# Kernel optimization log

Hardware: AMD Instinct MI355X
Metric: run time of the kernel (lower is better)

The kernel has to match this reference:

```python
import jax, jax.numpy as jnp
import numpy as np

SEQ, B, IN, H = 512, 256, 300, 256

def setup_inputs() -> dict:
    key = jax.random.key(0)
    ks = jax.random.split(key, 14)
    s = lambda *sh: 1.0 / np.sqrt(sh[0])
    inp = {
        'secuencia': jax.random.normal(ks[0], (SEQ, B, IN), jnp.float32),
        # RNN cell 1 (forward direction)
        'W1x': jax.random.normal(ks[1], (IN, H), jnp.float32) * s(IN),
        'W1h': jax.random.normal(ks[2], (H, H), jnp.float32) * s(H),
        'b1':  jax.random.normal(ks[3], (H,), jnp.float32) * 0.01,
        # RNN cell 2 (backward direction)
        'W2x': jax.random.normal(ks[4], (IN, H), jnp.float32) * s(IN),
        'W2h': jax.random.normal(ks[5], (H, H), jnp.float32) * s(H),
        'b2':  jax.random.normal(ks[6], (H,), jnp.float32) * 0.01,
        # MLP head (weights stored [in, out])
        'fc1_w': jax.random.normal(ks[7], (2 * H, 2 * H), jnp.float32) * s(2 * H),
        'fc1_b': jnp.zeros((2 * H,), jnp.float32),
        'fc2_w': jax.random.normal(ks[8], (2 * H, H), jnp.float32) * s(2 * H),
        'fc2_b': jnp.zeros((H,), jnp.float32),
        'fs_w':  jax.random.normal(ks[9], (H, 1), jnp.float32) * s(H),
        'fs_b':  jnp.zeros((1,), jnp.float32),
    }
    return inp

def _rnn_scan(seq, Wx, Wh, b):
    # seq: [S, B, IN] -> final hidden [B, H]; Elman cell h' = tanh(x Wx + h Wh + b)
    h0 = jnp.zeros((seq.shape[1], Wh.shape[0]), seq.dtype)
    def step(h, x):
        return jnp.tanh(x @ Wx + h @ Wh + b), None
    h_final, _ = jax.lax.scan(step, h0, seq)
    return h_final

def reference(secuencia, W1x, W1h, b1, W2x, W2h, b2,
              fc1_w, fc1_b, fc2_w, fc2_b, fs_w, fs_b):
    h1 = _rnn_scan(secuencia, W1x, W1h, b1)          # forward pass over time
    h2 = _rnn_scan(secuencia[::-1], W2x, W2h, b2)    # reversed pass over time
    h = jnp.concatenate([h1, h2], axis=1)            # [B, 2H]
    x = jax.nn.relu(h @ fc1_w + fc1_b)
    x = jax.nn.relu(x @ fc2_w + fc2_b)
    out = jnp.tanh(x @ fs_w + fs_b)                  # [B, 1]
    return out.squeeze()
```

## Files before the change

kernel.cpp:

```cpp
#include <hip/hip_runtime.h>

#define DI __device__ __forceinline__

typedef float f32x4 __attribute__((ext_vector_type(4)));
typedef float f4    __attribute__((ext_vector_type(4)));
typedef _Float16 h8 __attribute__((ext_vector_type(8)));
typedef _Float16 h4 __attribute__((ext_vector_type(4)));

#define SEQL 512
#define BATCH 256
#define INF 300
#define HID 256
#define N2 512
#define KP 320


DI float ftanh(float x) {
    float e = __builtin_amdgcn_exp2f(x * 2.8853900817779268f);
    return fmaf(-2.0f, __builtin_amdgcn_rcpf(e + 1.0f), 1.0f);
}

__global__ void prep_kernel(const float* __restrict__ W1x, const float* __restrict__ W2x,
                            const float* __restrict__ b1, const float* __restrict__ b2,
                            _Float16* __restrict__ WTs, float* __restrict__ bcat)
{
    int idx = blockIdx.x * 256 + threadIdx.x;
    if (idx < N2 * KP) {
        int j = idx / KP, z = idx - j * KP;
        int k = z ^ ((j & 7) << 3);
        float v = 0.f;
        if (k < INF) v = (j < HID) ? W1x[k * HID + j] : W2x[k * HID + (j - HID)];
        WTs[j * KP + z] = (_Float16)v;
    }
    if (idx < N2) bcat[idx] = (idx < HID) ? b1[idx] : b2[idx - HID];
}

__global__ __launch_bounds__(512, 2) void gemm_pre(
    const float* __restrict__ x, const _Float16* __restrict__ WTs,
    const float* __restrict__ bcat, _Float16* __restrict__ pre3)
{
    __shared__ _Float16 AbD[2][128 * 64];
    __shared__ _Float16 BbD[2][256 * 64];
    const int tid = threadIdx.x;
    const int w = tid >> 6, l = tid & 63;
    const int lj = l & 15, lg = l >> 4;
    const int bid = blockIdx.x;
    const int xcd = bid & 7;
    const int idx0 = bid >> 3;
    const int jn = idx0 & 1;
    const int bm = xcd * 128 + (idx0 >> 1);
    const size_t m0 = (size_t)bm * 128;
    const int j0b = jn * 256;
    const int wj = (w >> 1) * 64, wm2 = (w & 1) * 64;

    f32x4 acc[4][4];
#pragma unroll
    for (int a = 0; a < 4; ++a)
#pragma unroll
        for (int b = 0; b < 4; ++b) acc[a][b] = f32x4{0.f, 0.f, 0.f, 0.f};

    char* Acur = (char*)AbD[0];
    char* Anxt = (char*)AbD[1];
    char* Bcur = (char*)BbD[0];
    char* Bnxt = (char*)BbD[1];

    const int amr = w * 16;

#define STAGE_W(K0, BDST)                                                             \
    do {                                                                              \
        _Pragma("unroll")                                                             \
        for (int q = 0; q < 4; ++q) {                                                 \
            int idx = q * 512 + tid;                                                  \
            int jr = idx >> 3, sl = idx & 7;                                          \
            const _Float16* src = WTs + (size_t)(j0b + jr) * KP + (K0) + sl * 8;      \
            _Float16* dst = (_Float16*)(BDST) + (size_t)(q * 512 + w * 64) * 8;       \
            __builtin_amdgcn_global_load_lds(                                         \
                (const __attribute__((address_space(1))) void*)src,                   \
                (__attribute__((address_space(3))) void*)dst, 16, 0, 0);              \
        }                                                                             \
    } while (0)

#define LOAD_X(K0, XR)                                                                \
    do {                                                                              \
        _Pragma("unroll")                                                             \
        for (int c = 0; c < 4; ++c) {                                                 \
            int f = c * 512 + tid;                                                    \
            int mr = f >> 4, k4 = f & 15;                                             \
            if ((K0) + k4 * 4 + 3 < INF)                                              \
                XR[c] = *(const f4*)(x + (m0 + mr) * INF + (K0) + k4 * 4);            \
            else                                                                      \
                XR[c] = f4{0.f, 0.f, 0.f, 0.f};                                       \
        }                                                                             \
    } while (0)

#define WRITE_X(XR, ADST)                                                             \
    do {                                                                              \
        _Pragma("unroll")                                                             \
        for (int c = 0; c < 4; ++c) {                                                 \
            int f = c * 512 + tid;                                                    \
            int mr = f >> 4, k4 = f & 15;                                             \
            unsigned bo = (unsigned)mr * 128 + (((unsigned)k4 * 8) ^ ((mr & 7) << 4)); \
            *(h4*)((ADST) + bo) = h4{(_Float16)XR[c][0], (_Float16)XR[c][1],          \
                                     (_Float16)XR[c][2], (_Float16)XR[c][3]};         \
        }                                                                             \
    } while (0)

#define GBARRIER()                                                                    \
    do {                                                                              \
        __builtin_amdgcn_sched_barrier(0);                                            \
        asm volatile("s_waitcnt vmcnt(0) lgkmcnt(0)" ::: "memory");                   \
        __builtin_amdgcn_s_barrier();                                                 \
        __builtin_amdgcn_sched_barrier(0);                                            \
    } while (0)

    {
        f4 xr[4];
        STAGE_W(0, Bcur);
        LOAD_X(0, xr);
        asm volatile("s_waitcnt vmcnt(0)" ::: "memory");
        WRITE_X(xr, Acur);
        GBARRIER();
    }

    for (int s = 0; s < 5; ++s) {
        f4 xr[4];
        if (s < 4) {
            const int k0n = (s + 1) * 64;
            STAGE_W(k0n, Bnxt);
            LOAD_X(k0n, xr);
        }
#pragma unroll
        for (int kk = 0; kk < 2; ++kk) {
            h8 aw[4], bx[4];
#pragma unroll
            for (int jt = 0; jt < 4; ++jt) {
                int jr = wj + jt * 16 + lj;
                unsigned bo = (unsigned)jr * 128 + (((unsigned)(kk * 64 + lg * 16)) ^ ((jr & 7) << 4));
                aw[jt] = *(const h8*)(Bcur + bo);
            }
#pragma unroll
            for (int mt = 0; mt < 4; ++mt) {
                int mr = wm2 + mt * 16 + lj;
                unsigned bo = (unsigned)mr * 128 + (((unsigned)(kk * 64 + lg * 16)) ^ ((mr & 7) << 4));
                bx[mt] = *(const h8*)(Acur + bo);
            }
#pragma unroll
            for (int jt = 0; jt < 4; ++jt)
#pragma unroll
                for (int mt = 0; mt < 4; ++mt)
                    acc[jt][mt] = __builtin_amdgcn_mfma_f32_16x16x32_f16(aw[jt], bx[mt], acc[jt][mt], 0, 0, 0);
        }
        if (s < 4) {
            asm volatile("s_waitcnt vmcnt(0)" ::: "memory");
            WRITE_X(xr, Anxt);
        }
        GBARRIER();
        char* t0 = Acur; Acur = Anxt; Anxt = t0;
        char* t1 = Bcur; Bcur = Bnxt; Bnxt = t1;
    }
#undef STAGE_W
#undef LOAD_X
#undef WRITE_X
#undef GBARRIER

    f4 bias4[4];
#pragma unroll
    for (int jt = 0; jt < 4; ++jt)
        bias4[jt] = *(const f4*)(bcat + j0b + wj + jt * 16 + lg * 4);
    char* prc = (char*)pre3;
#pragma unroll
    for (int jt = 0; jt < 4; ++jt) {
        int slab = (j0b + wj + jt * 16) >> 4;
#pragma unroll
        for (int mt = 0; mt < 4; ++mt) {
            int M = (int)m0 + wm2 + mt * 16;
            size_t byte = (size_t)(M >> 8) * 262144 + (size_t)slab * 8192
                        + (size_t)((M & 255) + lj) * 32 + (size_t)lg * 8;
            h4 o;
#pragma unroll
            for (int i = 0; i < 4; ++i)
                o[i] = (_Float16)(acc[jt][mt][i] + bias4[jt][i]);
            *(h4*)(prc + byte) = o;
        }
    }
    (void)amr;
}

__global__ __launch_bounds__(512, 2) void rnn_scan(
    const float* __restrict__ W1h, const float* __restrict__ W2h,
    const _Float16* __restrict__ pre3, float* __restrict__ hcat)
{
    __shared__ char hbs[16384];
    char* hbc = hbs;
    const int tid = threadIdx.x;
    const int w = tid >> 6, l = tid & 63;
    const int lj = l & 15, lg = l >> 4;
    const int dir = blockIdx.x & 1;
    const int b0 = (int)(blockIdx.x >> 1) * 16;
    const float* Wh = dir ? W2h : W1h;
    const int j0 = w * 32;
    const int dirOff = dir ? HID : 0;

    h8 afrag[2][8];
#pragma unroll
    for (int jt = 0; jt < 2; ++jt) {
        int jc = j0 + jt * 16 + lj;
#pragma unroll
        for (int kk = 0; kk < 8; ++kk) {
            h8 t;
#pragma unroll
            for (int i = 0; i < 8; ++i) t[i] = (_Float16)Wh[(kk * 32 + lg * 8 + i) * HID + jc];
            afrag[jt][kk] = t;
        }
    }

    const unsigned rb = (unsigned)l * 16;
    const unsigned wb0 = (unsigned)w * 1024 + (unsigned)(lg >> 1) * 256
                       + (unsigned)lj * 16 + (unsigned)(lg & 1) * 8;

    ((h8*)hbs)[tid] = h8{0, 0, 0, 0, 0, 0, 0, 0};
    __syncthreads();

    const long long sb = dir ? -262144LL : 262144LL;
    const char* pp = (const char*)pre3 + (long long)(dir ? (SEQL - 1) : 0) * 262144
                   + (long long)dir * 131072
                   + (long long)w * 16384 + (long long)(b0 + lj) * 32 + lg * 8;
    h4 pA[2], pB[2];
#pragma unroll
    for (int jt = 0; jt < 2; ++jt) pA[jt] = *(const h4*)(pp + jt * 8192);
    pp += sb;
#pragma unroll
    for (int jt = 0; jt < 2; ++jt) pB[jt] = *(const h4*)(pp + jt * 8192);
    pp += sb;

#define RNN_STEP(RB, WB, P, DO_PF)                                                    \
    do {                                                                              \
        h8 bf[8];                                                                     \
        _Pragma("unroll")                                                             \
        for (int kk = 0; kk < 8; ++kk)                                                \
            bf[kk] = *(const h8*)(hbc + (RB) + kk * 1024 + rb);                       \
        f32x4 acc0, acc1;                                                             \
        _Pragma("unroll")                                                             \
        for (int i = 0; i < 4; ++i) { acc0[i] = (float)P[0][i]; acc1[i] = (float)P[1][i]; } \
        if (DO_PF) {                                                                  \
            P[0] = *(const h4*)(pp);                                                  \
            P[1] = *(const h4*)(pp + 8192);                                           \
            pp += sb;                                                                 \
        }                                                                             \
        _Pragma("unroll")                                                             \
        for (int kk = 0; kk < 8; ++kk)                                                \
            acc0 = __builtin_amdgcn_mfma_f32_16x16x32_f16(afrag[0][kk], bf[kk], acc0, 0, 0, 0); \
        h4 o0;                                                                        \
        _Pragma("unroll")                                                             \
        for (int i = 0; i < 4; ++i) o0[i] = (_Float16)ftanh(acc0[i]);                 \
        *(h4*)(hbc + (WB) + wb0) = o0;                                                \
        _Pragma("unroll")                                                             \
        for (int kk = 0; kk < 8; ++kk)                                                \
            acc1 = __builtin_amdgcn_mfma_f32_16x16x32_f16(afrag[1][kk], bf[kk], acc1, 0, 0, 0); \
        h4 o1;                                                                        \
        _Pragma("unroll")                                                             \
        for (int i = 0; i < 4; ++i) o1[i] = (_Float16)ftanh(acc1[i]);                 \
        *(h4*)(hbc + (WB) + wb0 + 512) = o1;                                          \
        __builtin_amdgcn_sched_barrier(0);                                            \
        asm volatile("s_waitcnt lgkmcnt(0)" ::: "memory");                            \
        __builtin_amdgcn_s_barrier();                                                 \
        __builtin_amdgcn_sched_barrier(0);                                            \
    } while (0)

    for (int tp = 0; tp < 255; ++tp) {
        RNN_STEP(0, 8192, pA, 1);
        RNN_STEP(8192, 0, pB, 1);
    }
    RNN_STEP(0, 8192, pA, 0);

    {
        f32x4 acc0, acc1;
#pragma unroll
        for (int i = 0; i < 4; ++i) { acc0[i] = (float)pB[0][i]; acc1[i] = (float)pB[1][i]; }
        h8 bf[8];
#pragma unroll
        for (int kk = 0; kk < 8; ++kk)
            bf[kk] = *(const h8*)(hbc + 8192 + kk * 1024 + rb);
#pragma unroll
        for (int kk = 0; kk < 8; ++kk) {
            acc0 = __builtin_amdgcn_mfma_f32_16x16x32_f16(afrag[0][kk], bf[kk], acc0, 0, 0, 0);
            acc1 = __builtin_amdgcn_mfma_f32_16x16x32_f16(afrag[1][kk], bf[kk], acc1, 0, 0, 0);
        }
        f4 v0, v1;
#pragma unroll
        for (int i = 0; i < 4; ++i) { v0[i] = ftanh(acc0[i]); v1[i] = ftanh(acc1[i]); }
        float* hc = hcat + (size_t)(b0 + lj) * N2 + dirOff + j0 + lg * 4;
        *(f4*)hc = v0;
        *(f4*)(hc + 16) = v1;
    }
#undef RNN_STEP
}

__global__ __launch_bounds__(256) void head_mlp(
    const float* __restrict__ hcat,
    const float* __restrict__ fc1w, const float* __restrict__ fc1b,
    const float* __restrict__ fc2w, const float* __restrict__ fc2b,
    const float* __restrict__ fsw, const float* __restrict__ fsb,
    float* __restrict__ out)
{
    __shared__ float hs[4 * 512];
    __shared__ float y1[4 * 512];
    __shared__ float y2[4 * 256];
    const int tid = threadIdx.x;
    const int b0 = blockIdx.x * 4;
    const int r = tid >> 6;
    const int lane = tid & 63;

#pragma unroll
    for (int c = 0; c < 2; ++c)
        ((f4*)hs)[c * 256 + tid] = ((const f4*)(hcat + (size_t)b0 * N2))[c * 256 + tid];
    __syncthreads();

    {
        const int j0 = lane * 8;
        f4 a0 = *(const f4*)(fc1b + j0);
        f4 a1 = *(const f4*)(fc1b + j0 + 4);
        for (int k = 0; k < 512; ++k) {
            float h = hs[r * 512 + k];
            f4 w0 = *(const f4*)(fc1w + (size_t)k * 512 + j0);
            f4 w1 = *(const f4*)(fc1w + (size_t)k * 512 + j0 + 4);
#pragma unroll
            for (int i = 0; i < 4; ++i) { a0[i] = fmaf(h, w0[i], a0[i]); a1[i] = fmaf(h, w1[i], a1[i]); }
        }
#pragma unroll
        for (int i = 0; i < 4; ++i) {
            y1[r * 512 + j0 + i]     = fmaxf(a0[i], 0.f);
            y1[r * 512 + j0 + 4 + i] = fmaxf(a1[i], 0.f);
        }
    }
    __syncthreads();

    {
        const int j2 = lane * 4;
        f4 a = *(const f4*)(fc2b + j2);
        for (int k = 0; k < 512; ++k) {
            float yv = y1[r * 512 + k];
            f4 w = *(const f4*)(fc2w + (size_t)k * 256 + j2);
#pragma unroll
            for (int i = 0; i < 4; ++i) a[i] = fmaf(yv, w[i], a[i]);
        }
#pragma unroll
        for (int i = 0; i < 4; ++i) y2[r * 256 + j2 + i] = fmaxf(a[i], 0.f);
    }
    __syncthreads();

    {
        float p = 0.f;
#pragma unroll
        for (int u = 0; u < 4; ++u)
            p = fmaf(y2[r * 256 + lane + u * 64], fsw[lane + u * 64], p);
#pragma unroll
        for (int off = 32; off > 0; off >>= 1) p += __shfl_down(p, off);
        __shared__ float red[4];
        if ((tid & 63) == 0) red[tid >> 6] = p;
        __syncthreads();
        if (tid == 0) {
            float s = red[0] + red[1] + red[2] + red[3];
        }
        if (lane == 0) out[b0 + r] = ftanh(p + fsb[0]);
    }
}

extern "C" void kernel_launch(void* const* d_in, const int* in_sizes, int n_in,
                              void* d_out, int out_size, void* d_ws, size_t ws_size,
                              hipStream_t stream)
{
    const float* x    = (const float*)d_in[0];
    const float* W1x  = (const float*)d_in[1];
    const float* W1h  = (const float*)d_in[2];
    const float* b1   = (const float*)d_in[3];
    const float* W2x  = (const float*)d_in[4];
    const float* W2h  = (const float*)d_in[5];
    const float* b2   = (const float*)d_in[6];
    const float* fc1w = (const float*)d_in[7];
    const float* fc1b = (const float*)d_in[8];
    const float* fc2w = (const float*)d_in[9];
    const float* fc2b = (const float*)d_in[10];
    const float* fsw  = (const float*)d_in[11];
    const float* fsb  = (const float*)d_in[12];

    char* ws = (char*)d_ws;
    size_t off = 0;
    _Float16* WTs  = (_Float16*)(ws + off); off += (size_t)N2 * KP * sizeof(_Float16);
    float* bcat    = (float*)(ws + off);    off += (size_t)N2 * sizeof(float);
    float* hcat    = (float*)(ws + off);    off += (size_t)BATCH * N2 * sizeof(float);
    _Float16* pre3 = (_Float16*)(ws + off); off += (size_t)SEQL * BATCH * N2 * sizeof(_Float16);
    if (off > ws_size) return;

    prep_kernel<<<(N2 * KP + 255) / 256, 256, 0, stream>>>(W1x, W2x, b1, b2, WTs, bcat);
    gemm_pre<<<2048, 512, 0, stream>>>(x, WTs, bcat, pre3);
    rnn_scan<<<(BATCH / 16) * 2, 512, 0, stream>>>(W1h, W2h, pre3, hcat);
    head_mlp<<<64, 256, 0, stream>>>(hcat, fc1w, fc1b, fc2w, fc2b, fsw, fsb, (float*)d_out);
}
```

Baseline: 476.5 us.

## Fuse input-projection GEMM and RNN scan into one kernel with flag-based overlap

Merges the input-projection GEMM and the recurrent scan into one persistent launch. The first 32 blocks run the scan, while the remaining blocks compute the projection in an order that alternates from both ends of the sequence. Each GEMM block bumps a per-group counter, and scan blocks spin on these counters so the serial scan can start before the whole GEMM finishes. This hides GEMM time behind the latency-bound recurrence. In exchange it adds spin-wait polling, atomic loads and a deeper prefetch of four steps, and it depends on the scan blocks being co-resident with GEMM blocks that make progress.

Measured after the change: 524.0 us. 1.1x slower.

```diff
diff --git a/kernel.cpp b/kernel.cpp
--- a/kernel.cpp
+++ b/kernel.cpp
@@ -13,6 +13,8 @@
 #define HID 256
 #define N2 512
 #define KP 320
+#define RNN_BLOCKS 32
+#define GEMM_BLOCKS 2048
 
 
 DI float ftanh(float x) {
@@ -20,9 +22,16 @@
     return fmaf(-2.0f, __builtin_amdgcn_rcpf(e + 1.0f), 1.0f);
 }
 
+DI h4 ald8(const void* p) {
+    unsigned long long u = __hip_atomic_load((const unsigned long long*)p,
+                                             __ATOMIC_RELAXED, __HIP_MEMORY_SCOPE_AGENT);
+    union { unsigned long long u; h4 h; } c; c.u = u; return c.h;
+}
+
 __global__ void prep_kernel(const float* __restrict__ W1x, const float* __restrict__ W2x,
                             const float* __restrict__ b1, const float* __restrict__ b2,
-                            _Float16* __restrict__ WTs, float* __restrict__ bcat)
+                            _Float16* __restrict__ WTs, float* __restrict__ bcat,
+                            unsigned* __restrict__ gflags)
 {
     int idx = blockIdx.x * 256 + threadIdx.x;
     if (idx < N2 * KP) {
@@ -33,38 +42,43 @@
         WTs[j * KP + z] = (_Float16)v;
     }
     if (idx < N2) bcat[idx] = (idx < HID) ? b1[idx] : b2[idx - HID];
-}
-
-__global__ __launch_bounds__(512, 2) void gemm_pre(
+    if (idx < 64) gflags[idx] = 0u;
+}
+
+__global__ __launch_bounds__(512, 1) void fused_kernel(
     const float* __restrict__ x, const _Float16* __restrict__ WTs,
-    const float* __restrict__ bcat, _Float16* __restrict__ pre3)
+    const float* __restrict__ bcat,
+    const float* __restrict__ W1h, const float* __restrict__ W2h,
+    _Float16* __restrict__ pre3, float* __restrict__ hcat,
+    unsigned* __restrict__ gflags)
 {
-    __shared__ _Float16 AbD[2][128 * 64];
-    __shared__ _Float16 BbD[2][256 * 64];
+    __shared__ char smem[98304];
     const int tid = threadIdx.x;
     const int w = tid >> 6, l = tid & 63;
     const int lj = l & 15, lg = l >> 4;
-    const int bid = blockIdx.x;
-    const int xcd = bid & 7;
-    const int idx0 = bid >> 3;
-    const int jn = idx0 & 1;
-    const int bm = xcd * 128 + (idx0 >> 1);
-    const size_t m0 = (size_t)bm * 128;
-    const int j0b = jn * 256;
-    const int wj = (w >> 1) * 64, wm2 = (w & 1) * 64;
-
-    f32x4 acc[4][4];
-#pragma unroll
-    for (int a = 0; a < 4; ++a)
-#pragma unroll
-        for (int b = 0; b < 4; ++b) acc[a][b] = f32x4{0.f, 0.f, 0.f, 0.f};
-
-    char* Acur = (char*)AbD[0];
-    char* Anxt = (char*)AbD[1];
-    char* Bcur = (char*)BbD[0];
-    char* Bnxt = (char*)BbD[1];
-
-    const int amr = w * 16;
+
+    if (blockIdx.x >= RNN_BLOCKS) {
+        char* A0 = smem;
+        char* A1 = smem + 16384;
+        char* B0 = smem + 32768;
+        char* B1 = smem + 65536;
+        const int g = blockIdx.x - RNN_BLOCKS;
+        const int k4i = g >> 2, r = g & 3;
+        const int t = (k4i & 1) ? (511 - (k4i >> 1)) : (k4i >> 1);
+        const int bm = 2 * t + (r >> 1);
+        const int jn = r & 1;
+        const size_t m0 = (size_t)bm * 128;
+        const int j0b = jn * 256;
+        const int wj = (w >> 1) * 64, wm2 = (w & 1) * 64;
+
+        f32x4 acc[4][4];
+#pragma unroll
+        for (int a = 0; a < 4; ++a)
+#pragma unroll
+            for (int b = 0; b < 4; ++b) acc[a][b] = f32x4{0.f, 0.f, 0.f, 0.f};
+
+        char* Acur = A0; char* Anxt = A1;
+        char* Bcur = B0; char* Bnxt = B1;
 
 #define STAGE_W(K0, BDST)                                                             \
     do {                                                                              \
@@ -113,88 +127,82 @@
         __builtin_amdgcn_sched_barrier(0);                                            \
     } while (0)
 
-    {
-        f4 xr[4];
-        STAGE_W(0, Bcur);
-        LOAD_X(0, xr);
-        asm volatile("s_waitcnt vmcnt(0)" ::: "memory");
-        WRITE_X(xr, Acur);
-        GBARRIER();
-    }
-
-    for (int s = 0; s < 5; ++s) {
-        f4 xr[4];
-        if (s < 4) {
-            const int k0n = (s + 1) * 64;
-            STAGE_W(k0n, Bnxt);
-            LOAD_X(k0n, xr);
-        }
-#pragma unroll
-        for (int kk = 0; kk < 2; ++kk) {
-            h8 aw[4], bx[4];
-#pragma unroll
-            for (int jt = 0; jt < 4; ++jt) {
-                int jr = wj + jt * 16 + lj;
-                unsigned bo = (unsigned)jr * 128 + (((unsigned)(kk * 64 + lg * 16)) ^ ((jr & 7) << 4));
-                aw[jt] = *(const h8*)(Bcur + bo);
+        {
+            f4 xr[4];
+            STAGE_W(0, Bcur);
+            LOAD_X(0, xr);
+            asm volatile("s_waitcnt vmcnt(0)" ::: "memory");
+            WRITE_X(xr, Acur);
+            GBARRIER();
+        }
+        for (int s = 0; s < 5; ++s) {
+            f4 xr[4];
+            if (s < 4) {
+                const int k0n = (s + 1) * 64;
+                STAGE_W(k0n, Bnxt);
+                LOAD_X(k0n, xr);
             }
 #pragma unroll
-            for (int mt = 0; mt < 4; ++mt) {
-                int mr = wm2 + mt * 16 + lj;
-                unsigned bo = (unsigned)mr * 128 + (((unsigned)(kk * 64 + lg * 16)) ^ ((mr & 7) << 4));
-                bx[mt] = *(const h8*)(Acur + bo);
+            for (int kk = 0; kk < 2; ++kk) {
+                h8 aw[4], bx[4];
+#pragma unroll
+                for (int jt = 0; jt < 4; ++jt) {
+                    int jr = wj + jt * 16 + lj;
+                    unsigned bo = (unsigned)jr * 128 + (((unsigned)(kk * 64 + lg * 16)) ^ ((jr & 7) << 4));
+                    aw[jt] = *(const h8*)(Bcur + bo);
+                }
+#pragma unroll
+                for (int mt = 0; mt < 4; ++mt) {
+                    int mr = wm2 + mt * 16 + lj;
+                    unsigned bo = (unsigned)mr * 128 + (((unsigned)(kk * 64 + lg * 16)) ^ ((mr & 7) << 4));
+                    bx[mt] = *(const h8*)(Acur + bo);
+                }
+#pragma unroll
+                for (int jt = 0; jt < 4; ++jt)
+#pragma unroll
+                    for (int mt = 0; mt < 4; ++mt)
+                        acc[jt][mt] = __builtin_amdgcn_mfma_f32_16x16x32_f16(aw[jt], bx[mt], acc[jt][mt], 0, 0, 0);
             }
-#pragma unroll
-            for (int jt = 0; jt < 4; ++jt)
-#pragma unroll
-                for (int mt = 0; mt < 4; ++mt)
-                    acc[jt][mt] = __builtin_amdgcn_mfma_f32_16x16x32_f16(aw[jt], bx[mt], acc[jt][mt], 0, 0, 0);
-        }
-        if (s < 4) {
-            asm volatile("s_waitcnt vmcnt(0)" ::: "memory");
-            WRITE_X(xr, Anxt);
-        }
-        GBARRIER();
-        char* t0 = Acur; Acur = Anxt; Anxt = t0;
-        char* t1 = Bcur; Bcur = Bnxt; Bnxt = t1;
-    }
+            if (s < 4) {
+                asm volatile("s_waitcnt vmcnt(0)" ::: "memory");
+                WRITE_X(xr, Anxt);
+            }
+            GBARRIER();
+            char* t0 = Acur; Acur = Anxt; Anxt = t0;
+            char* t1 = Bcur; Bcur = Bnxt; Bnxt = t1;
+        }
 #undef STAGE_W
 #undef LOAD_X
 #undef WRITE_X
 #undef GBARRIER
-
-    f4 bias4[4];
-#pragma unroll
-    for (int jt = 0; jt < 4; ++jt)
-        bias4[jt] = *(const f4*)(bcat + j0b + wj + jt * 16 + lg * 4);
-    char* prc = (char*)pre3;
-#pragma unroll
-    for (int jt = 0; jt < 4; ++jt) {
-        int slab = (j0b + wj + jt * 16) >> 4;
-#pragma unroll
-        for (int mt = 0; mt < 4; ++mt) {
-            int M = (int)m0 + wm2 + mt * 16;
-            size_t byte = (size_t)(M >> 8) * 262144 + (size_t)slab * 8192
-                        + (size_t)((M & 255) + lj) * 32 + (size_t)lg * 8;
-            h4 o;
-#pragma unroll
-            for (int i = 0; i < 4; ++i)
-                o[i] = (_Float16)(acc[jt][mt][i] + bias4[jt][i]);
-            *(h4*)(prc + byte) = o;
-        }
-    }
-    (void)amr;
-}
-
-__global__ __launch_bounds__(512, 2) void rnn_scan(
-    const float* __restrict__ W1h, const float* __restrict__ W2h,
-    const _Float16* __restrict__ pre3, float* __restrict__ hcat)
-{
-    __shared__ char hbs[16384];
-    char* hbc = hbs;
-    const int tid = threadIdx.x;
-    const int w = tid >> 6, l = tid & 63;
-    const int lj = l & 15, lg = l >> 4;
+        f4 bias4[4];
+#pragma unroll
+        for (int jt = 0; jt < 4; ++jt)
+            bias4[jt] = *(const f4*)(bcat + j0b + wj + jt * 16 + lg * 4);
+        char* prc = (char*)pre3;
+#pragma unroll
+        for (int jt = 0; jt < 4; ++jt) {
+            int slab = (j0b + wj + jt * 16) >> 4;
+#pragma unroll
+            for (int mt = 0; mt < 4; ++mt) {
+                int M = (int)m0 + wm2 + mt * 16;
+                size_t byte = (size_t)(M >> 8) * 262144 + (size_t)slab * 8192
+                            + (size_t)((M & 255) + lj) * 32 + (size_t)lg * 8;
+                h4 o;
+#pragma unroll
+                for (int i = 0; i < 4; ++i)
+                    o[i] = (_Float16)(acc[jt][mt][i] + bias4[jt][i]);
+                *(h4*)(prc + byte) = o;
+            }
+        }
+        __syncthreads();
+        if (tid == 0)
+            __hip_atomic_fetch_add(&gflags[t >> 3], 1u, __ATOMIC_RELEASE, __HIP_MEMORY_SCOPE_AGENT);
+        return;
+    }
+
+    __builtin_amdgcn_s_setprio(2);
+    char* hbc = smem;
     const int dir = blockIdx.x & 1;
     const int b0 = (int)(blockIdx.x >> 1) * 16;
     const float* Wh = dir ? W2h : W1h;
@@ -207,10 +215,10 @@
         int jc = j0 + jt * 16 + lj;
 #pragma unroll
         for (int kk = 0; kk < 8; ++kk) {
-            h8 t;
-#pragma unroll
-            for (int i = 0; i < 8; ++i) t[i] = (_Float16)Wh[(kk * 32 + lg * 8 + i) * HID + jc];
-            afrag[jt][kk] = t;
+            h8 tr;
+#pragma unroll
+            for (int i = 0; i < 8; ++i) tr[i] = (_Float16)Wh[(kk * 32 + lg * 8 + i) * HID + jc];
+            afrag[jt][kk] = tr;
         }
     }
 
@@ -218,20 +226,27 @@
     const unsigned wb0 = (unsigned)w * 1024 + (unsigned)(lg >> 1) * 256
                        + (unsigned)lj * 16 + (unsigned)(lg & 1) * 8;
 
-    ((h8*)hbs)[tid] = h8{0, 0, 0, 0, 0, 0, 0, 0};
+    ((h8*)hbc)[tid] = h8{0, 0, 0, 0, 0, 0, 0, 0};
     __syncthreads();
+
+#define WAITG(G)                                                                      \
+    while (__hip_atomic_load(&gflags[(G)], __ATOMIC_ACQUIRE, __HIP_MEMORY_SCOPE_AGENT) < 32u) \
+        __builtin_amdgcn_s_sleep(8)
+
+    const int G0 = dir ? 63 : 0;
+    const int gstep = dir ? -1 : 1;
+    WAITG(G0);
+    WAITG(G0 + gstep);
 
     const long long sb = dir ? -262144LL : 262144LL;
     const char* pp = (const char*)pre3 + (long long)(dir ? (SEQL - 1) : 0) * 262144
                    + (long long)dir * 131072
                    + (long long)w * 16384 + (long long)(b0 + lj) * 32 + lg * 8;
-    h4 pA[2], pB[2];
-#pragma unroll
-    for (int jt = 0; jt < 2; ++jt) pA[jt] = *(const h4*)(pp + jt * 8192);
-    pp += sb;
-#pragma unroll
-    for (int jt = 0; jt < 2; ++jt) pB[jt] = *(const h4*)(pp + jt * 8192);
-    pp += sb;
+    h4 P0[2], P1[2], P2[2], P3[2];
+    P0[0] = ald8(pp); P0[1] = ald8(pp + 8192); pp += sb;
+    P1[0] = ald8(pp); P1[1] = ald8(pp + 8192); pp += sb;
+    P2[0] = ald8(pp); P2[1] = ald8(pp + 8192); pp += sb;
+    P3[0] = ald8(pp); P3[1] = ald8(pp + 8192); pp += sb;
 
 #define RNN_STEP(RB, WB, P, DO_PF)                                                    \
     do {                                                                              \
@@ -243,8 +258,8 @@
         _Pragma("unroll")                                                             \
         for (int i = 0; i < 4; ++i) { acc0[i] = (float)P[0][i]; acc1[i] = (float)P[1][i]; } \
         if (DO_PF) {                                                                  \
-            P[0] = *(const h4*)(pp);                                                  \
-            P[1] = *(const h4*)(pp + 8192);                                           \
+            P[0] = ald8(pp);                                                          \
+            P[1] = ald8(pp + 8192);                                                   \
             pp += sb;                                                                 \
         }                                                                             \
         _Pragma("unroll")                                                             \
@@ -267,16 +282,25 @@
         __builtin_amdgcn_sched_barrier(0);                                            \
     } while (0)
 
-    for (int tp = 0; tp < 255; ++tp) {
-        RNN_STEP(0, 8192, pA, 1);
-        RNN_STEP(8192, 0, pB, 1);
-    }
-    RNN_STEP(0, 8192, pA, 0);
-
+    for (int q = 0; q < 126; ++q) {
+        if (q & 1) { WAITG(G0 + gstep * ((q + 1) >> 1)); }
+        RNN_STEP(0, 8192, P0, 1);
+        RNN_STEP(8192, 0, P1, 1);
+        RNN_STEP(0, 8192, P2, 1);
+        RNN_STEP(8192, 0, P3, 1);
+    }
+    WAITG(G0 + gstep * 63);
+    RNN_STEP(0, 8192, P0, 1);
+    RNN_STEP(8192, 0, P1, 1);
+    RNN_STEP(0, 8192, P2, 1);
+    RNN_STEP(8192, 0, P3, 1);
+    RNN_STEP(0, 8192, P0, 0);
+    RNN_STEP(8192, 0, P1, 0);
+    RNN_STEP(0, 8192, P2, 0);
     {
         f32x4 acc0, acc1;
 #pragma unroll
-        for (int i = 0; i < 4; ++i) { acc0[i] = (float)pB[0][i]; acc1[i] = (float)pB[1][i]; }
+        for (int i = 0; i < 4; ++i) { acc0[i] = (float)P3[0][i]; acc1[i] = (float)P3[1][i]; }
         h8 bf[8];
 #pragma unroll
         for (int kk = 0; kk < 8; ++kk)
@@ -294,6 +318,7 @@
         *(f4*)(hc + 16) = v1;
     }
 #undef RNN_STEP
+#undef WAITG
 }
 
 __global__ __launch_bounds__(256) void head_mlp(
@@ -356,12 +381,6 @@
             p = fmaf(y2[r * 256 + lane + u * 64], fsw[lane + u * 64], p);
 #pragma unroll
         for (int off = 32; off > 0; off >>= 1) p += __shfl_down(p, off);
-        __shared__ float red[4];
-        if ((tid & 63) == 0) red[tid >> 6] = p;
-        __syncthreads();
-        if (tid == 0) {
-            float s = red[0] + red[1] + red[2] + red[3];
-        }
         if (lane == 0) out[b0 + r] = ftanh(p + fsb[0]);
     }
 }
@@ -386,14 +405,15 @@
 
     char* ws = (char*)d_ws;
     size_t off = 0;
-    _Float16* WTs  = (_Float16*)(ws + off); off += (size_t)N2 * KP * sizeof(_Float16);
-    float* bcat    = (float*)(ws + off);    off += (size_t)N2 * sizeof(float);
-    float* hcat    = (float*)(ws + off);    off += (size_t)BATCH * N2 * sizeof(float);
-    _Float16* pre3 = (_Float16*)(ws + off); off += (size_t)SEQL * BATCH * N2 * sizeof(_Float16);
+    _Float16* WTs    = (_Float16*)(ws + off); off += (size_t)N2 * KP * sizeof(_Float16);
+    float* bcat      = (float*)(ws + off);    off += (size_t)N2 * sizeof(float);
+    float* hcat      = (float*)(ws + off);    off += (size_t)BATCH * N2 * sizeof(float);
+    unsigned* gflags = (unsigned*)(ws + off); off += 4096;
+    _Float16* pre3   = (_Float16*)(ws + off); off += (size_t)SEQL * BATCH * N2 * sizeof(_Float16);
     if (off > ws_size) return;
 
-    prep_kernel<<<(N2 * KP + 255) / 256, 256, 0, stream>>>(W1x, W2x, b1, b2, WTs, bcat);
-    gemm_pre<<<2048, 512, 0, stream>>>(x, WTs, bcat, pre3);
-    rnn_scan<<<(BATCH / 16) * 2, 512, 0, stream>>>(W1h, W2h, pre3, hcat);
+    prep_kernel<<<(N2 * KP + 255) / 256, 256, 0, stream>>>(W1x, W2x, b1, b2, WTs, bcat, gflags);
+    fused_kernel<<<RNN_BLOCKS + GEMM_BLOCKS, 512, 0, stream>>>(
+        x, WTs, bcat, W1h, W2h, pre3, hcat, gflags);
     head_mlp<<<64, 256, 0, stream>>>(hcat, fc1w, fc1b, fc2w, fc2b, fsw, fsb, (float*)d_out);
 }
```
